# Performance work log

Hardware: AMD Instinct MI355X
Metric: run time of the kernel (lower is better)

## Reference

```python
import jax, jax.numpy as jnp
import numpy as np

N = 50000   # nodes
E = 800000  # edges (before self-loops)
IN_C, HID, OUT_C = 10, 96, 48


def setup_inputs() -> dict:
    key = jax.random.key(0)
    ks = jax.random.split(key, 8)
    x = jax.random.normal(ks[0], (N, IN_C), dtype=jnp.float32)
    edge_index = jax.random.randint(ks[1], (2, E), 0, N, dtype=jnp.int64)
    # Glorot-ish scaled weights for the three GCN layers
    W1 = jax.random.normal(ks[2], (IN_C, HID), dtype=jnp.float32) * (1.0 / np.sqrt(IN_C))
    b1 = jnp.zeros((HID,), dtype=jnp.float32)
    W_mu = jax.random.normal(ks[3], (HID, OUT_C), dtype=jnp.float32) * (1.0 / np.sqrt(HID))
    b_mu = jnp.zeros((OUT_C,), dtype=jnp.float32)
    W_logstd = jax.random.normal(ks[4], (HID, OUT_C), dtype=jnp.float32) * (1.0 / np.sqrt(HID))
    b_logstd = jnp.zeros((OUT_C,), dtype=jnp.float32)
    return {"x": x, "edge_index": edge_index, "W1": W1, "b1": b1,
            "W_mu": W_mu, "b_mu": b_mu, "W_logstd": W_logstd, "b_logstd": b_logstd}


def _gcn_norm(edge_index, n_nodes, dtype):
    # PyG gcn_norm: add self-loops, symmetric normalization D^-1/2 A D^-1/2
    loops = jnp.arange(n_nodes, dtype=edge_index.dtype)
    ei = jnp.concatenate([edge_index, jnp.stack([loops, loops])], axis=1)
    row, col = ei[0], ei[1]
    deg = jax.ops.segment_sum(jnp.ones(ei.shape[1], dtype=dtype), col, num_segments=n_nodes)
    dis = jnp.where(deg > 0, jax.lax.rsqrt(deg), jnp.zeros_like(deg))
    norm = dis[row] * dis[col]  # [E+N]
    return row, col, norm


def _gcn_conv(h, row, col, norm, W, b, n_nodes):
    hw = h @ W                                   # dense projection [N, F_out]
    msgs = hw[row] * norm[:, None]               # gather + scale   [E+N, F_out]
    out = jax.ops.segment_sum(msgs, col, num_segments=n_nodes)  # scatter-add
    return out + b


def reference(x, edge_index, W1, b1, W_mu, b_mu, W_logstd, b_logstd):
    row, col, norm = _gcn_norm(edge_index, N, x.dtype)
    h = jax.nn.relu(_gcn_conv(x, row, col, norm, W1, b1, N))
    mu = _gcn_conv(h, row, col, norm, W_mu, b_mu, N)
    logstd = _gcn_conv(h, row, col, norm, W_logstd, b_logstd, N)
    return mu, logstd
```

## Files before the change

kernel.cpp:

```cpp
#include <hip/hip_runtime.h>
#include <hip/hip_bf16.h>

#define NND 50000
#define NED 800000
#define INC 10
#define HID 96
#define OUTC 48
#define NOUT (NND*OUTC)
#define MTILES 3125
#define NW 98
#define SPAN 512
#define EW_CAP 9216
#define PB 200
#define PBE 4000

typedef __hip_bfloat16 bf16;
typedef __attribute__((ext_vector_type(8))) short short8;
typedef __attribute__((ext_vector_type(4))) float f32x4;

#define W1F_O  0L
#define B1F_O  960L
#define BMF_O  1056L
#define BLF_O  1104L
#define DIS_O  1152L
#define XS_O   51152L
#define FLOATS_TOT 551152L

__device__ __forceinline__ float b2f(bf16 v) { return __bfloat162float(v); }
__device__ __forceinline__ float bfLo(unsigned int p) { return __uint_as_float(p << 16); }
__device__ __forceinline__ float bfHi(unsigned int p) { return __uint_as_float(p & 0xffff0000u); }
__device__ __forceinline__ unsigned short f2bu(float v) {
    return __bfloat16_as_ushort(__float2bfloat16(v));
}

__global__ __launch_bounds__(256) void k_part(const int* ei, const void* x,
                                              const void* w1, const void* b1,
                                              const void* wm, const void* bm,
                                              const void* wl, const void* bl,
                                              int* flags, float* F, unsigned short* wct,
                                              unsigned int* part, int* smat, int* cmat) {
    __shared__ int s_oddnz, s_big;
    __shared__ int counts[NW], cur[NW];
    __shared__ unsigned int buf[PBE];
    int tid = threadIdx.x;
    if (tid == 0) { s_oddnz = 0; s_big = 0; }
    for (int i = tid; i < NW; i += 256) counts[i] = 0;
    __syncthreads();
    {
        if (tid < 128) {
            if (ei[2 * tid + 1] != 0) atomicOr(&s_oddnz, 1);
        }
        const unsigned short* xs = (const unsigned short*)x;
        unsigned short u = xs[tid * 8];
        float f = __uint_as_float(((unsigned int)u) << 16);
        int big = !(fabsf(f) < 64.0f);
        unsigned short u2 = xs[tid * 8 + 5];
        float f2 = __uint_as_float(((unsigned int)u2) << 16);
        big |= !(fabsf(f2) < 64.0f);
        if (big) atomicOr(&s_big, 1);
    }
    __syncthreads();
    int iw = (s_oddnz == 0) ? 1 : 0;
    int ff = s_big ? 1 : 0;
    if (blockIdx.x == 0 && tid == 0) { flags[0] = iw; flags[1] = ff; }

    if (blockIdx.x < 41) {
        int idx = blockIdx.x * 256 + tid;
        if (idx < 10368) {
            const void* src; long off; int mode; long dst = 0;
            if      (idx < 960)  { src = w1; off = idx;        mode = 0; dst = W1F_O + idx; }
            else if (idx < 1056) { src = b1; off = idx - 960;  mode = 0; dst = B1F_O + (idx - 960); }
            else if (idx < 1104) { src = bm; off = idx - 1056; mode = 0; dst = BMF_O + (idx - 1056); }
            else if (idx < 1152) { src = bl; off = idx - 1104; mode = 0; dst = BLF_O + (idx - 1104); }
            else if (idx < 5760) { src = wm; off = idx - 1152; mode = 1; }
            else                 { src = wl; off = idx - 5760; mode = 2; }
            float v = ff ? ((const float*)src)[off] : b2f(((const bf16*)src)[off]);
            if (mode == 0) F[dst] = v;
            else if (mode == 1) wct[(off % OUTC) * (long)HID + off / OUTC] = f2bu(v);
            else                wct[(OUTC + off % OUTC) * (long)HID + off / OUTC] = f2bu(v);
        }
    }

    unsigned int wreg[16];
    int base = blockIdx.x * 1000;
    for (int it = 0; it < 4; ++it) {
        int j = it * 256 + tid;
        if (j < 1000) {
            int j4 = base + j;
            int r0, r1, r2, r3, c0, c1, c2, c3;
            if (iw) {
                const int4* pr = (const int4*)ei;
                const int4* pc = (const int4*)(ei + 2L * NED);
                int4 ra = pr[2 * j4], rb = pr[2 * j4 + 1];
                int4 ca = pc[2 * j4], cb = pc[2 * j4 + 1];
                r0 = ra.x; r1 = ra.z; r2 = rb.x; r3 = rb.z;
                c0 = ca.x; c1 = ca.z; c2 = cb.x; c3 = cb.z;
            } else {
                int4 ra = ((const int4*)ei)[j4];
                int4 ca = ((const int4*)(ei + NED))[j4];
                r0 = ra.x; r1 = ra.y; r2 = ra.z; r3 = ra.w;
                c0 = ca.x; c1 = ca.y; c2 = ca.z; c3 = ca.w;
            }
            wreg[4 * it]     = (unsigned)r0 | ((unsigned)c0 << 16);
            wreg[4 * it + 1] = (unsigned)r1 | ((unsigned)c1 << 16);
            wreg[4 * it + 2] = (unsigned)r2 | ((unsigned)c2 << 16);
            wreg[4 * it + 3] = (unsigned)r3 | ((unsigned)c3 << 16);
            atomicAdd(&counts[wreg[4 * it]     >> 25], 1);
            atomicAdd(&counts[wreg[4 * it + 1] >> 25], 1);
            atomicAdd(&counts[wreg[4 * it + 2] >> 25], 1);
            atomicAdd(&counts[wreg[4 * it + 3] >> 25], 1);
        }
    }
    __syncthreads();
    if (tid < NW) {
        int run = 0;
        for (int j = 0; j < tid; ++j) run += counts[j];
        cur[tid] = run;
        cmat[tid * PB + blockIdx.x] = counts[tid];
        smat[tid * PB + blockIdx.x] = blockIdx.x * PBE + run;
    }
    __syncthreads();
    for (int it = 0; it < 4; ++it) {
        int j = it * 256 + tid;
        if (j < 1000) {
#pragma unroll
            for (int q = 0; q < 4; ++q) {
                unsigned int w = wreg[4 * it + q];
                int pos = atomicAdd(&cur[w >> 25], 1);
                buf[pos] = w;
            }
        }
    }
    __syncthreads();
    for (int i = tid; i < PBE; i += 256) part[blockIdx.x * PBE + i] = buf[i];
}

__global__ __launch_bounds__(1024) void k_win(const unsigned int* part, const int* smat,
                                              const int* cmat, const void* x, float* F,
                                              int* cnt, int* start, unsigned short* csr) {
    __shared__ int Lrun[PB], Srun[PB];
    __shared__ int hist[SPAN], st[SPAN], cur[SPAN];
    __shared__ float dl[SPAN];
    __shared__ int s_big;
    int tid = threadIdx.x;
    int w = blockIdx.x;
    if (tid == 0) s_big = 0;
    if (tid < PB) { Lrun[tid] = cmat[w * PB + tid]; Srun[tid] = smat[w * PB + tid]; }
    if (tid < SPAN) hist[tid] = 0;
    __syncthreads();
    if (tid < 256) {
        const unsigned short* xs = (const unsigned short*)x;
        unsigned short u = xs[tid * 8];
        float f = __uint_as_float(((unsigned int)u) << 16);
        int big = !(fabsf(f) < 64.0f);
        unsigned short u2 = xs[tid * 8 + 5];
        float f2 = __uint_as_float(((unsigned int)u2) << 16);
        big |= !(fabsf(f2) < 64.0f);
        if (big) atomicOr(&s_big, 1);
    }
    unsigned int lo = (unsigned)w * SPAN;
    int wave = tid >> 6, lane = tid & 63;
    for (int rb = wave; rb < PB; rb += 16) {
        int L = Lrun[rb], S = Srun[rb];
        for (int i = lane; i < L; i += 64)
            atomicAdd(&hist[(part[S + i] >> 16) - lo], 1);
    }
    __syncthreads();
    int ff = s_big;
    if (tid < SPAN) st[tid] = hist[tid];
    __syncthreads();
    for (int off = 1; off < SPAN; off <<= 1) {
        int t = (tid < SPAN && tid >= off) ? st[tid - off] : 0;
        __syncthreads();
        if (tid < SPAN) st[tid] += t;
        __syncthreads();
    }
    if (tid < SPAN) {
        int h0 = hist[tid];
        int abs0 = w * EW_CAP + (st[tid] - h0);
        cur[tid] = abs0;
        float dis = rsqrtf((float)h0 + 1.0f);
        dl[tid] = dis;
        int g = (int)lo + tid;
        if (g < NND) {
            cnt[g] = h0; start[g] = abs0;
            F[DIS_O + g] = dis;
        }
    }
    __syncthreads();
    for (int i = tid; i < SPAN * INC; i += 1024) {
        int node = (int)lo + i / INC;
        if (node < NND) {
            long xo = (long)node * INC + (i % INC);
            float xv = ff ? ((const float*)x)[xo] : b2f(((const bf16*)x)[xo]);
            F[XS_O + xo] = dl[i / INC] * xv;
        }
    }
    int lim = (w + 1) * EW_CAP;
    for (int rb = wave; rb < PB; rb += 16) {
        int L = Lrun[rb], S = Srun[rb];
        for (int i = lane; i < L; i += 64) {
            unsigned int e = part[S + i];
            int pos = atomicAdd(&cur[(e >> 16) - lo], 1);
            if (pos < lim) csr[pos] = (unsigned short)(e & 0xffffu);
        }
    }
}

__global__ __launch_bounds__(256) void k_layer1(const int* cnt, const int* start,
                                                const unsigned short* csr, const float* F,
                                                unsigned short* h) {
    __shared__ float w1s[1056];
    for (int i = threadIdx.x; i < 1056; i += 256) w1s[i] = F[W1F_O + i];
    __syncthreads();
    int idx = blockIdx.x * 256 + threadIdx.x;
    if (idx >= NND * 4) return;
    int node = idx >> 2, sub = idx & 3;
    int s = start[node], t = s + cnt[node];
    int lim = ((node >> 9) + 1) * EW_CAP;
    if (t > lim) t = lim;
    float ax[INC];
#pragma unroll
    for (int j = 0; j < INC; ++j) ax[j] = 0.0f;
    for (int k = s + sub; k < t; k += 4) {
        int src = csr[k];
        const float2* xr = (const float2*)(F + XS_O + (long)src * INC);
#pragma unroll
        for (int j = 0; j < 5; ++j) {
            float2 v = xr[j];
            ax[2 * j]     += v.x;
            ax[2 * j + 1] += v.y;
        }
    }
    if (sub == 0) {
        const float2* xr = (const float2*)(F + XS_O + (long)node * INC);
#pragma unroll
        for (int j = 0; j < 5; ++j) {
            float2 v = xr[j];
            ax[2 * j]     += v.x;
            ax[2 * j + 1] += v.y;
        }
    }
#pragma unroll
    for (int j = 0; j < INC; ++j) {
        ax[j] += __shfl_xor(ax[j], 1, 64);
        ax[j] += __shfl_xor(ax[j], 2, 64);
    }
    float dn = F[DIS_O + node];
#pragma unroll
    for (int j = 0; j < INC; ++j) ax[j] *= dn;
    int f0 = sub * 24;
    unsigned int* hrow = (unsigned int*)(h + (size_t)node * HID);
#pragma unroll
    for (int f = f0; f < f0 + 24; f += 2) {
        float a0 = w1s[960 + f], a1 = w1s[960 + f + 1];
#pragma unroll
        for (int kk = 0; kk < INC; ++kk) {
            a0 = fmaf(ax[kk], w1s[kk * HID + f], a0);
            a1 = fmaf(ax[kk], w1s[kk * HID + f + 1], a1);
        }
        a0 = fmaxf(a0, 0.0f) * dn;
        a1 = fmaxf(a1, 0.0f) * dn;
        unsigned int u0 = f2bu(a0), u1 = f2bu(a1);
        hrow[f >> 1] = u0 | (u1 << 16);
    }
}

__global__ __launch_bounds__(256) void k_gh(const int* cnt, const int* start,
                                            const unsigned short* csr, const float* F,
                                            const unsigned short* h, const unsigned short* wct,
                                            const int* flags, void* dout) {
    int wid = threadIdx.x >> 6;
    int lane = threadIdx.x & 63;
    int mtile = blockIdx.x * 4 + wid;
    if (mtile >= MTILES) return;
    int l16 = lane & 15, quad = lane >> 4;
    int node = mtile * 16 + l16;

    const uint4* hb4 = (const uint4*)h;
    long rowq = (long)node * 12;

    int s = start[node], c = cnt[node];
    int lim = ((node >> 9) + 1) * EW_CAP;
    if (s + c > lim) c = lim - s;

    float acc[3][8];
    {
        uint4 p0 = hb4[rowq + quad];
        uint4 p1 = hb4[rowq + 4 + quad];
        uint4 p2 = hb4[rowq + 8 + quad];
#pragma unroll
        for (int t = 0; t < 4; ++t) {
            unsigned int w0 = (t == 0) ? p0.x : (t == 1) ? p0.y : (t == 2) ? p0.z : p0.w;
            unsigned int w1 = (t == 0) ? p1.x : (t == 1) ? p1.y : (t == 2) ? p1.z : p1.w;
            unsigned int w2 = (t == 0) ? p2.x : (t == 1) ? p2.y : (t == 2) ? p2.z : p2.w;
            acc[0][2 * t] = bfLo(w0); acc[0][2 * t + 1] = bfHi(w0);
            acc[1][2 * t] = bfLo(w1); acc[1][2 * t + 1] = bfHi(w1);
            acc[2][2 * t] = bfLo(w2); acc[2][2 * t + 1] = bfHi(w2);
        }
    }
    int k = 0;
    for (; k + 1 < c; k += 2) {
        int s0 = csr[s + k], s1 = csr[s + k + 1];
        long r0 = (long)s0 * 12, r1 = (long)s1 * 12;
        uint4 a0 = hb4[r0 + quad], a1 = hb4[r0 + 4 + quad], a2 = hb4[r0 + 8 + quad];
        uint4 b0 = hb4[r1 + quad], b1 = hb4[r1 + 4 + quad], b2 = hb4[r1 + 8 + quad];
#pragma unroll
        for (int t = 0; t < 4; ++t) {
            unsigned int w0 = (t == 0) ? a0.x : (t == 1) ? a0.y : (t == 2) ? a0.z : a0.w;
            unsigned int w1 = (t == 0) ? a1.x : (t == 1) ? a1.y : (t == 2) ? a1.z : a1.w;
            unsigned int w2 = (t == 0) ? a2.x : (t == 1) ? a2.y : (t == 2) ? a2.z : a2.w;
            acc[0][2 * t] += bfLo(w0); acc[0][2 * t + 1] += bfHi(w0);
            acc[1][2 * t] += bfLo(w1); acc[1][2 * t + 1] += bfHi(w1);
            acc[2][2 * t] += bfLo(w2); acc[2][2 * t + 1] += bfHi(w2);
        }
#pragma unroll
        for (int t = 0; t < 4; ++t) {
            unsigned int w0 = (t == 0) ? b0.x : (t == 1) ? b0.y : (t == 2) ? b0.z : b0.w;
            unsigned int w1 = (t == 0) ? b1.x : (t == 1) ? b1.y : (t == 2) ? b1.z : b1.w;
            unsigned int w2 = (t == 0) ? b2.x : (t == 1) ? b2.y : (t == 2) ? b2.z : b2.w;
            acc[0][2 * t] += bfLo(w0); acc[0][2 * t + 1] += bfHi(w0);
            acc[1][2 * t] += bfLo(w1); acc[1][2 * t + 1] += bfHi(w1);
            acc[2][2 * t] += bfLo(w2); acc[2][2 * t + 1] += bfHi(w2);
        }
    }
    if (k < c) {
        int s0 = csr[s + k];
        long r0 = (long)s0 * 12;
        uint4 a0 = hb4[r0 + quad], a1 = hb4[r0 + 4 + quad], a2 = hb4[r0 + 8 + quad];
#pragma unroll
        for (int t = 0; t < 4; ++t) {
            unsigned int w0 = (t == 0) ? a0.x : (t == 1) ? a0.y : (t == 2) ? a0.z : a0.w;
            unsigned int w1 = (t == 0) ? a1.x : (t == 1) ? a1.y : (t == 2) ? a1.z : a1.w;
            unsigned int w2 = (t == 0) ? a2.x : (t == 1) ? a2.y : (t == 2) ? a2.z : a2.w;
            acc[0][2 * t] += bfLo(w0); acc[0][2 * t + 1] += bfHi(w0);
            acc[1][2 * t] += bfLo(w1); acc[1][2 * t + 1] += bfHi(w1);
            acc[2][2 * t] += bfLo(w2); acc[2][2 * t + 1] += bfHi(w2);
        }
    }
    float dn = F[DIS_O + node];
    short8 af[3];
#pragma unroll
    for (int g = 0; g < 3; ++g)
#pragma unroll
        for (int j = 0; j < 8; ++j)
            af[g][j] = (short)f2bu(acc[g][j] * dn);

    int ff = flags[1];
#pragma unroll
    for (int nt = 0; nt < 6; ++nt) {
        const unsigned short* wb = wct + ((size_t)nt * 16 + l16) * HID + quad * 8;
        short8 b0 = *(const short8*)(wb);
        short8 b1 = *(const short8*)(wb + 32);
        short8 b2 = *(const short8*)(wb + 64);
        f32x4 cacc = {0.0f, 0.0f, 0.0f, 0.0f};
        cacc = __builtin_amdgcn_mfma_f32_16x16x32_bf16(af[0], b0, cacc, 0, 0, 0);
        cacc = __builtin_amdgcn_mfma_f32_16x16x32_bf16(af[1], b1, cacc, 0, 0, 0);
        cacc = __builtin_amdgcn_mfma_f32_16x16x32_bf16(af[2], b2, cacc, 0, 0, 0);
        int n = nt * 16 + l16;
        float bias = (n < OUTC) ? F[BMF_O + n] : F[BLF_O + n - OUTC];
        long obase = (n < OUTC) ? ((long)n) : (NOUT + (long)(n - OUTC));
#pragma unroll
        for (int r = 0; r < 4; ++r) {
            int m = mtile * 16 + quad * 4 + r;
            float val = cacc[r] + bias;
            long oi = (long)m * OUTC + obase;
            if (ff) ((float*)dout)[oi] = val;
            else    ((bf16*)dout)[oi] = __float2bfloat16(val);
        }
    }
}

extern "C" void kernel_launch(void* const* d_in, const int* in_sizes, int n_in,
                              void* d_out, int out_size, void* d_ws, size_t ws_size,
                              hipStream_t stream) {
    const int* ei = (const int*)d_in[1];
    int* flags = (int*)d_ws;
    float* F = (float*)((char*)d_ws + 256);
    unsigned short* h   = (unsigned short*)(F + FLOATS_TOT);
    unsigned short* wct = h + (size_t)NND * HID;
    int* cnt   = (int*)(wct + (size_t)HID * HID);
    int* start = cnt + NND;
    unsigned int* part = (unsigned int*)(start + NND);
    int* smat = (int*)(part + NED);
    int* cmat = smat + NW * PB;
    unsigned short* csr = (unsigned short*)(cmat + NW * PB);

    k_part<<<PB, 256, 0, stream>>>(ei, d_in[0], d_in[2], d_in[3], d_in[4],
                                   d_in[5], d_in[6], d_in[7], flags, F, wct,
                                   part, smat, cmat);
    k_win<<<NW, 1024, 0, stream>>>(part, smat, cmat, d_in[0], F, cnt, start, csr);
    k_layer1<<<(NND * 4 + 255) / 256, 256, 0, stream>>>(cnt, start, csr, F, h);
    k_gh<<<(MTILES + 3) / 4, 256, 0, stream>>>(cnt, start, csr, F, h, wct, flags, d_out);
}
```

Before: 149.9 us.

## Sort nodes by in-degree within each window to balance wave work

Builds a per-window permutation that groups nodes by in-degree using a counting sort in shared memory. The layer-1 and fused gather/MFMA kernels then process nodes in this order, so lanes in a wave have similar neighbour counts and less loop divergence. Output rows are scattered through the permutation. The cost is an extra indirection, less contiguous h row and output writes, and a small serial prefix scan in k_win.

```diff
diff --git a/kernel.cpp b/kernel.cpp
--- a/kernel.cpp
+++ b/kernel.cpp
@@ -137,16 +137,19 @@
 
 __global__ __launch_bounds__(1024) void k_win(const unsigned int* part, const int* smat,
                                               const int* cmat, const void* x, float* F,
-                                              int* cnt, int* start, unsigned short* csr) {
+                                              int* cnt, int* start, unsigned short* csr,
+                                              int* perm) {
     __shared__ int Lrun[PB], Srun[PB];
     __shared__ int hist[SPAN], st[SPAN], cur[SPAN];
     __shared__ float dl[SPAN];
+    __shared__ int dh[64];
     __shared__ int s_big;
     int tid = threadIdx.x;
     int w = blockIdx.x;
     if (tid == 0) s_big = 0;
     if (tid < PB) { Lrun[tid] = cmat[w * PB + tid]; Srun[tid] = smat[w * PB + tid]; }
     if (tid < SPAN) hist[tid] = 0;
+    if (tid < 64) dh[tid] = 0;
     __syncthreads();
     if (tid < 256) {
         const unsigned short* xs = (const unsigned short*)x;
@@ -188,6 +191,28 @@
         }
     }
     __syncthreads();
+    if (tid < SPAN) {
+        int g = (int)lo + tid;
+        if (g < NND) {
+            int b = hist[tid]; if (b > 63) b = 63;
+            atomicAdd(&dh[b], 1);
+        }
+    }
+    __syncthreads();
+    if (tid == 0) {
+        int run = 0;
+#pragma unroll 1
+        for (int i = 0; i < 64; ++i) { int c = dh[i]; dh[i] = run; run += c; }
+    }
+    __syncthreads();
+    if (tid < SPAN) {
+        int g = (int)lo + tid;
+        if (g < NND) {
+            int b = hist[tid]; if (b > 63) b = 63;
+            int rk = atomicAdd(&dh[b], 1);
+            perm[w * SPAN + rk] = g;
+        }
+    }
     for (int i = tid; i < SPAN * INC; i += 1024) {
         int node = (int)lo + i / INC;
         if (node < NND) {
@@ -209,13 +234,14 @@
 
 __global__ __launch_bounds__(256) void k_layer1(const int* cnt, const int* start,
                                                 const unsigned short* csr, const float* F,
-                                                unsigned short* h) {
+                                                const int* perm, unsigned short* h) {
     __shared__ float w1s[1056];
     for (int i = threadIdx.x; i < 1056; i += 256) w1s[i] = F[W1F_O + i];
     __syncthreads();
     int idx = blockIdx.x * 256 + threadIdx.x;
     if (idx >= NND * 4) return;
-    int node = idx >> 2, sub = idx & 3;
+    int rank = idx >> 2, sub = idx & 3;
+    int node = perm[rank];
     int s = start[node], t = s + cnt[node];
     int lim = ((node >> 9) + 1) * EW_CAP;
     if (t > lim) t = lim;
@@ -269,13 +295,13 @@
 __global__ __launch_bounds__(256) void k_gh(const int* cnt, const int* start,
                                             const unsigned short* csr, const float* F,
                                             const unsigned short* h, const unsigned short* wct,
-                                            const int* flags, void* dout) {
+                                            const int* perm, const int* flags, void* dout) {
     int wid = threadIdx.x >> 6;
     int lane = threadIdx.x & 63;
     int mtile = blockIdx.x * 4 + wid;
     if (mtile >= MTILES) return;
     int l16 = lane & 15, quad = lane >> 4;
-    int node = mtile * 16 + l16;
+    int node = perm[mtile * 16 + l16];
 
     const uint4* hb4 = (const uint4*)h;
     long rowq = (long)node * 12;
@@ -345,6 +371,10 @@
 #pragma unroll
         for (int j = 0; j < 8; ++j)
             af[g][j] = (short)f2bu(acc[g][j] * dn);
+
+    int pm[4];
+#pragma unroll
+    for (int r = 0; r < 4; ++r) pm[r] = perm[mtile * 16 + quad * 4 + r];
 
     int ff = flags[1];
 #pragma unroll
@@ -362,7 +392,7 @@
         long obase = (n < OUTC) ? ((long)n) : (NOUT + (long)(n - OUTC));
 #pragma unroll
         for (int r = 0; r < 4; ++r) {
-            int m = mtile * 16 + quad * 4 + r;
+            int m = pm[r];
             float val = cacc[r] + bias;
             long oi = (long)m * OUTC + obase;
             if (ff) ((float*)dout)[oi] = val;
@@ -385,11 +415,12 @@
     int* smat = (int*)(part + NED);
     int* cmat = smat + NW * PB;
     unsigned short* csr = (unsigned short*)(cmat + NW * PB);
+    int* perm = (int*)(csr + (size_t)NW * EW_CAP);
 
     k_part<<<PB, 256, 0, stream>>>(ei, d_in[0], d_in[2], d_in[3], d_in[4],
                                    d_in[5], d_in[6], d_in[7], flags, F, wct,
                                    part, smat, cmat);
-    k_win<<<NW, 1024, 0, stream>>>(part, smat, cmat, d_in[0], F, cnt, start, csr);
-    k_layer1<<<(NND * 4 + 255) / 256, 256, 0, stream>>>(cnt, start, csr, F, h);
-    k_gh<<<(MTILES + 3) / 4, 256, 0, stream>>>(cnt, start, csr, F, h, wct, flags, d_out);
-}
+    k_win<<<NW, 1024, 0, stream>>>(part, smat, cmat, d_in[0], F, cnt, start, csr, perm);
+    k_layer1<<<(NND * 4 + 255) / 256, 256, 0, stream>>>(cnt, start, csr, F, perm, h);
+    k_gh<<<(MTILES + 3) / 4, 256, 0, stream>>>(cnt, start, csr, F, h, wct, perm, flags, d_out);
+}
```

New measurement: 167.3 us. 11.6% more time.
